# Optimization experiments

Measured on AMD Instinct MI355X. Metric: run time of the kernel, lower is better.

Reference implementation:

```python
import jax, jax.numpy as jnp
import numpy as np

B, S, HID = 4, 2048, 1024
H, DH = 16, 64  # HID = H * DH
ADP, NTASKS = 64, 10
GATE_S = 100.0  # s (soft gate temperature), != smax=400 so no hard threshold


def setup_inputs() -> dict:
    key = jax.random.key(0)
    ks = jax.random.split(key, 13)
    sc = 0.02
    return {
        "hidden_states": jax.random.normal(ks[0], (B, S, HID), jnp.float32),
        "Wq": jax.random.normal(ks[1], (HID, HID), jnp.float32) * sc,
        "bq": jax.random.normal(ks[2], (HID,), jnp.float32) * sc,
        "Wk": jax.random.normal(ks[3], (HID, HID), jnp.float32) * sc,
        "bk": jax.random.normal(ks[4], (HID,), jnp.float32) * sc,
        "Wv": jax.random.normal(ks[5], (HID, HID), jnp.float32) * sc,
        "bv": jax.random.normal(ks[6], (HID,), jnp.float32) * sc,
        "fc1_w": jax.random.normal(ks[7], (HID, ADP), jnp.float32) * sc,
        "fc1_b": jax.random.normal(ks[8], (ADP,), jnp.float32) * sc,
        "fc2_w": jax.random.normal(ks[9], (ADP, HID), jnp.float32) * sc,
        "fc2_b": jax.random.normal(ks[10], (HID,), jnp.float32) * sc,
        "efc1": jax.random.normal(ks[11], (NTASKS, ADP), jnp.float32),
        "efc2": jax.random.normal(ks[12], (NTASKS, HID), jnp.float32),
        "t": 3,
    }


def reference(hidden_states, Wq, bq, Wk, bk, Wv, bv,
              fc1_w, fc1_b, fc2_w, fc2_b, efc1, efc2, t):
    x = hidden_states
    # --- parallel adapter with task gates (add_residual=False) ---
    gfc1 = jax.nn.sigmoid(GATE_S * efc1[t])  # [ADP]
    gfc2 = jax.nn.sigmoid(GATE_S * efc2[t])  # [HID]
    h = jax.nn.relu(x @ fc1_w + fc1_b) * gfc1          # [B,S,ADP]
    adapter_out = jax.nn.relu(h @ fc2_w + fc2_b) * gfc2  # [B,S,HID]
    # --- multi-head self-attention (absolute positions, no mask, eval dropout) ---
    def split_heads(y):  # [B,S,HID] -> [B,H,S,DH]
        return y.reshape(B, S, H, DH).transpose(0, 2, 1, 3)
    q = split_heads(x @ Wq + bq)
    k = split_heads(x @ Wk + bk)
    v = split_heads(x @ Wv + bv)
    scores = jnp.einsum("bhqd,bhkd->bhqk", q, k) / np.sqrt(DH).astype(jnp.float32)
    probs = jax.nn.softmax(scores, axis=-1)
    ctx = jnp.einsum("bhqk,bhkd->bhqd", probs, v)
    ctx = ctx.transpose(0, 2, 1, 3).reshape(B, S, HID)
    return ctx + adapter_out
```

## Files before the change

kernel.cpp:

```cpp
#include <hip/hip_runtime.h>
#include <stdint.h>
#include <stddef.h>

typedef unsigned short u16;
typedef unsigned int u32;
typedef __bf16 bf16x8 __attribute__((ext_vector_type(8)));
typedef __bf16 bf16x4 __attribute__((ext_vector_type(4)));
typedef short s16x4 __attribute__((ext_vector_type(4)));
typedef float f32x4 __attribute__((ext_vector_type(4)));

#define BB  4
#define SS  2048
#define HIDD 1024
#define NH  16
#define DHD 64

#define GLD16(gaddr, laddr) \
  __builtin_amdgcn_global_load_lds( \
      (const __attribute__((address_space(1))) u32*)(gaddr), \
      (__attribute__((address_space(3))) u32*)(laddr), 16, 0, 0)

#define LDS_BARRIER() asm volatile("s_waitcnt lgkmcnt(0)\n\ts_barrier" ::: "memory")

#if __has_builtin(__builtin_amdgcn_exp2f)
  #define EXP2(x) __builtin_amdgcn_exp2f(x)
#else
  #define EXP2(x) __expf((x) * 0.6931471805599453f)
#endif

__device__ __forceinline__ u16 f2b(float f){
  union { float f; unsigned u; } c; c.f = f;
  unsigned r = c.u + 0x7fffu + ((c.u >> 16) & 1u);
  return (u16)(r >> 16);
}
__device__ __forceinline__ f32x4 mfma32(bf16x8 a, bf16x8 b, f32x4 c){
  return __builtin_amdgcn_mfma_f32_16x16x32_bf16(a, b, c, 0, 0, 0);
}
__device__ __forceinline__ f32x4 mfma16(s16x4 a, s16x4 b, f32x4 c){
  return __builtin_amdgcn_mfma_f32_16x16x16bf16_1k(a, b, c, 0, 0, 0);
}

__global__ __launch_bounds__(256)
void prep(const float* __restrict__ x, u16* __restrict__ xb,
          const float* __restrict__ Wq, const float* __restrict__ Wk,
          const float* __restrict__ Wv, const float* __restrict__ f1w,
          const float* __restrict__ f2w,
          u16* __restrict__ wqkv, u16* __restrict__ wtf1, u16* __restrict__ wtf2)
{
  __shared__ float tile[32][33];
  int blk = blockIdx.x;
  const int tid = threadIdx.x;
  if (blk < 8192) {
    int i = blk * 1024 + tid * 4;
    float4 v = *reinterpret_cast<const float4*>(&x[i]);
    ushort4 o;
    o.x = f2b(v.x); o.y = f2b(v.y); o.z = f2b(v.z); o.w = f2b(v.w);
    *reinterpret_cast<ushort4*>(&xb[i]) = o;
    return;
  }
  blk -= 8192;
  if (blk >= 3200) {
    u16* pad = wqkv + (size_t)3136 * 1024;
    uint4 z = make_uint4(0u, 0u, 0u, 0u);
    *reinterpret_cast<uint4*>(&pad[(size_t)(blk - 3200) * 2048 + tid * 8]) = z;
    return;
  }
  const float* in; u16* out; int R, C, c0, r0;
  if (blk < 3072) {
    int m = blk >> 10, t = blk & 1023;
    in = (m == 0) ? Wq : (m == 1) ? Wk : Wv;
    out = wqkv + (size_t)m * 1024 * 1024;
    R = 1024; C = 1024; c0 = (t & 31) * 32; r0 = (t >> 5) * 32;
  } else if (blk < 3136) {
    int t = blk - 3072;
    in = f1w; out = wtf1; R = 1024; C = 64;
    c0 = (t & 1) * 32; r0 = (t >> 1) * 32;
  } else {
    int t = blk - 3136;
    in = f2w; out = wtf2; R = 64; C = 1024;
    c0 = (t & 31) * 32; r0 = (t >> 5) * 32;
  }
  int tx = tid & 31, ty = tid >> 5;
  #pragma unroll
  for (int j = 0; j < 32; j += 8)
    tile[ty + j][tx] = in[(size_t)(r0 + ty + j) * C + c0 + tx];
  __syncthreads();
  #pragma unroll
  for (int j = 0; j < 32; j += 8)
    out[(size_t)(c0 + ty + j) * R + r0 + tx] = f2b(tile[tx][ty + j]);
}

__global__ __launch_bounds__(256)
void gemm_qkv(const u16* __restrict__ X, const u16* __restrict__ Wt,
              const float* __restrict__ bq, const float* __restrict__ bk,
              const float* __restrict__ bv,
              const float* __restrict__ f1b, const float* __restrict__ efc1,
              const int* __restrict__ tptr,
              u16* __restrict__ qb, u16* __restrict__ kb, u16* __restrict__ vt,
              u16* __restrict__ hb)
{
  constexpr int K = 1024;
  __shared__ __align__(16) u16 ldsX[128 * 32];
  __shared__ __align__(16) u16 ldsW[128 * 32];
  const int tid = threadIdx.x;
  const int w = tid >> 6, lane = tid & 63, quad = lane >> 4, ln = lane & 15;
  const int m0 = blockIdx.y * 128, n0 = blockIdx.x * 128;
  const int wrow = (w >> 1) * 64;
  const int wcol = (w & 1) * 64;
  const int srow = tid >> 2;
  const int scol = (tid & 3) * 8;

  f32x4 acc[4][4] = {};

  for (int k0 = 0; k0 < K; k0 += 32) {
    #pragma unroll
    for (int c = 0; c < 2; ++c)
      GLD16(&X[(size_t)(m0 + c * 64 + srow) * K + k0 + scol], &ldsX[c * 2048 + w * 512]);
    #pragma unroll
    for (int c = 0; c < 2; ++c)
      GLD16(&Wt[(size_t)(n0 + c * 64 + srow) * K + k0 + scol], &ldsW[c * 2048 + w * 512]);
    __syncthreads();

    bf16x8 a[4], bfr[4];
    #pragma unroll
    for (int mt = 0; mt < 4; ++mt)
      a[mt] = *reinterpret_cast<const bf16x8*>(&ldsX[(wrow + mt * 16 + ln) * 32 + quad * 8]);
    #pragma unroll
    for (int nt = 0; nt < 4; ++nt)
      bfr[nt] = *reinterpret_cast<const bf16x8*>(&ldsW[(wcol + nt * 16 + ln) * 32 + quad * 8]);
    #pragma unroll
    for (int mt = 0; mt < 4; ++mt)
      #pragma unroll
      for (int nt = 0; nt < 4; ++nt)
        acc[mt][nt] = mfma32(a[mt], bfr[nt], acc[mt][nt]);
    __syncthreads();
  }

  if (n0 < 2048) {
    const float scale = (n0 < 1024) ? 0.18033688f : 1.f;
    const float* bias = (n0 < 1024) ? bq : bk;
    u16* dst = (n0 < 1024) ? qb : kb;
    const int nb = n0 & 1023;
    #pragma unroll
    for (int nt = 0; nt < 4; ++nt) {
      const int col = nb + wcol + nt * 16 + ln;
      const float bvv = bias[col];
      #pragma unroll
      for (int mt = 0; mt < 4; ++mt)
        #pragma unroll
        for (int r = 0; r < 4; ++r) {
          int row = m0 + wrow + mt * 16 + quad * 4 + r;
          dst[(size_t)row * 1024 + col] = f2b((acc[mt][nt][r] + bvv) * scale);
        }
    }
  } else if (n0 < 3072) {
    #pragma unroll
    for (int nt = 0; nt < 4; ++nt) {
      const int colv = (n0 - 2048) + wcol + nt * 16 + ln;
      const float bvv = bv[colv];
      const int h = colv >> 6, d = colv & 63;
      #pragma unroll
      for (int mt = 0; mt < 4; ++mt) {
        int row = m0 + wrow + mt * 16 + quad * 4;
        int bb = row >> 11, s = row & 2047;
        ushort4 o;
        o.x = f2b(acc[mt][nt][0] + bvv);
        o.y = f2b(acc[mt][nt][1] + bvv);
        o.z = f2b(acc[mt][nt][2] + bvv);
        o.w = f2b(acc[mt][nt][3] + bvv);
        *reinterpret_cast<ushort4*>(
            &vt[((((size_t)bb * NH + h) * DHD + d) << 11) + s]) = o;
      }
    }
  } else if (wcol == 0) {
    int t = tptr[0];
    if ((unsigned)t > 9u) t = 0;
    #pragma unroll
    for (int nt = 0; nt < 4; ++nt) {
      const int col = nt * 16 + ln;
      const float bvv = f1b[col];
      const float g = 1.f / (1.f + __expf(-100.f * efc1[t * 64 + col]));
      #pragma unroll
      for (int mt = 0; mt < 4; ++mt)
        #pragma unroll
        for (int r = 0; r < 4; ++r) {
          int row = m0 + wrow + mt * 16 + quad * 4 + r;
          hb[(size_t)row * 64 + col] = f2b(fmaxf(acc[mt][nt][r] + bvv, 0.f) * g);
        }
    }
  }
}

__global__ __launch_bounds__(256, 4)
void attn(const u16* __restrict__ Q, const u16* __restrict__ Kb,
          const u16* __restrict__ Vt, const u16* __restrict__ hb,
          const u16* __restrict__ w2, const float* __restrict__ b2,
          const float* __restrict__ gate2, const int* __restrict__ tptr,
          float* __restrict__ out)
{
  __shared__ __align__(16) u16 ldsK[64 * 72];
  __shared__ __align__(16) u16 ldsV[64 * 76];

  const int tid = threadIdx.x;
  const int w = tid >> 6, lane = tid & 63, quad = lane >> 4, ln = lane & 15;
  const int h = blockIdx.x, b = blockIdx.y, qt = blockIdx.z;
  const int bh = b * NH + h;
  const int qbase = qt * 128 + w * 32;
  const int skey = tid >> 3;
  const int sd   = (tid & 7) * 8;

  bf16x8 qf[2][2];
  #pragma unroll
  for (int q2 = 0; q2 < 2; ++q2)
    #pragma unroll
    for (int kk = 0; kk < 2; ++kk)
      qf[q2][kk] = *reinterpret_cast<const bf16x8*>(
          &Q[(size_t)(b * SS + qbase + q2 * 16 + ln) * HIDD + h * DHD + kk * 32 + quad * 8]);

  f32x4 o[4][2] = {};
  f32x4 lacc[2] = {};
  const s16x4 ones = {0x3F80, 0x3F80, 0x3F80, 0x3F80};

  const u16* Kp = &Kb[(size_t)(b * SS + skey) * HIDD + h * DHD + sd];
  const u16* Vp = &Vt[((size_t)bh * DHD + skey) * SS + sd];

  uint4 rK0 = *reinterpret_cast<const uint4*>(Kp);
  uint4 rK1 = *reinterpret_cast<const uint4*>(Kp + (size_t)32 * HIDD);
  uint4 rV0 = *reinterpret_cast<const uint4*>(Vp);
  uint4 rV1 = *reinterpret_cast<const uint4*>(Vp + (size_t)32 * SS);

  for (int kt = 0; kt < SS; kt += 64) {
    LDS_BARRIER();
    *reinterpret_cast<uint4*>(&ldsK[skey * 72 + sd])        = rK0;
    *reinterpret_cast<uint4*>(&ldsK[(32 + skey) * 72 + sd]) = rK1;
    *reinterpret_cast<uint4*>(&ldsV[skey * 76 + sd])        = rV0;
    *reinterpret_cast<uint4*>(&ldsV[(32 + skey) * 76 + sd]) = rV1;
    if (kt + 64 < SS) {
      const u16* Kn = Kp + (size_t)(kt + 64) * HIDD;
      const u16* Vn = Vp + (kt + 64);
      rK0 = *reinterpret_cast<const uint4*>(Kn);
      rK1 = *reinterpret_cast<const uint4*>(Kn + (size_t)32 * HIDD);
      rV0 = *reinterpret_cast<const uint4*>(Vn);
      rV1 = *reinterpret_cast<const uint4*>(Vn + (size_t)32 * SS);
    }
    LDS_BARRIER();

    f32x4 s[4][2];
    __builtin_amdgcn_s_setprio(1);
    #pragma unroll
    for (int k4 = 0; k4 < 4; ++k4) {
      bf16x8 kf0 = *reinterpret_cast<const bf16x8*>(&ldsK[(k4 * 16 + ln) * 72 + quad * 8]);
      bf16x8 kf1 = *reinterpret_cast<const bf16x8*>(&ldsK[(k4 * 16 + ln) * 72 + 32 + quad * 8]);
      #pragma unroll
      for (int q2 = 0; q2 < 2; ++q2) {
        f32x4 z = {0.f, 0.f, 0.f, 0.f};
        z = mfma32(kf0, qf[q2][0], z);
        z = mfma32(kf1, qf[q2][1], z);
        s[k4][q2] = z;
      }
    }
    __builtin_amdgcn_s_setprio(0);

    s16x4 p[4][2];
    #pragma unroll
    for (int k4 = 0; k4 < 4; ++k4)
      #pragma unroll
      for (int q2 = 0; q2 < 2; ++q2) {
        union { bf16x4 b; s16x4 s; } cv;
        #pragma unroll
        for (int r = 0; r < 4; ++r)
          cv.b[r] = (__bf16)EXP2(s[k4][q2][r]);
        p[k4][q2] = cv.s;
      }

    __builtin_amdgcn_s_setprio(1);
    #pragma unroll
    for (int dt = 0; dt < 4; ++dt) {
      #pragma unroll
      for (int ks = 0; ks < 4; ++ks) {
        s16x4 vf = *reinterpret_cast<const s16x4*>(
            &ldsV[(dt * 16 + ln) * 76 + ks * 16 + quad * 4]);
        #pragma unroll
        for (int q2 = 0; q2 < 2; ++q2)
          o[dt][q2] = mfma16(vf, p[ks][q2], o[dt][q2]);
      }
    }
    #pragma unroll
    for (int ks = 0; ks < 4; ++ks)
      #pragma unroll
      for (int q2 = 0; q2 < 2; ++q2)
        lacc[q2] = mfma16(ones, p[ks][q2], lacc[q2]);
    __builtin_amdgcn_s_setprio(0);
  }

  float rl[2];
  #pragma unroll
  for (int q2 = 0; q2 < 2; ++q2)
    rl[q2] = 1.f / lacc[q2][0];

  f32x4 acc2[4][2] = {};
  #pragma unroll
  for (int kk = 0; kk < 2; ++kk) {
    bf16x8 hf[2];
    #pragma unroll
    for (int q2 = 0; q2 < 2; ++q2) {
      int q = qbase + q2 * 16 + ln;
      hf[q2] = *reinterpret_cast<const bf16x8*>(
          &hb[(size_t)(b * SS + q) * 64 + kk * 32 + quad * 8]);
    }
    #pragma unroll
    for (int dt = 0; dt < 4; ++dt) {
      bf16x8 wf = *reinterpret_cast<const bf16x8*>(
          &w2[(size_t)(h * DHD + dt * 16 + ln) * 64 + kk * 32 + quad * 8]);
      #pragma unroll
      for (int q2 = 0; q2 < 2; ++q2)
        acc2[dt][q2] = mfma32(wf, hf[q2], acc2[dt][q2]);
    }
  }

  int t = tptr[0];
  if ((unsigned)t > 9u) t = 0;
  float bv2[4][4], gv2[4][4];
  #pragma unroll
  for (int dt = 0; dt < 4; ++dt)
    #pragma unroll
    for (int r = 0; r < 4; ++r) {
      int col = h * DHD + dt * 16 + quad * 4 + r;
      bv2[dt][r] = b2[col];
      gv2[dt][r] = 1.f / (1.f + __expf(-100.f * gate2[t * HIDD + col]));
    }

  #pragma unroll
  for (int q2 = 0; q2 < 2; ++q2) {
    const int q = qbase + q2 * 16 + ln;
    float* orow = &out[(size_t)(b * SS + q) * HIDD + h * DHD];
    #pragma unroll
    for (int dt = 0; dt < 4; ++dt)
      #pragma unroll
      for (int r = 0; r < 4; ++r) {
        int d = dt * 16 + quad * 4 + r;
        float ad = fmaxf(acc2[dt][q2][r] + bv2[dt][r], 0.f) * gv2[dt][r];
        orow[d] = o[dt][q2][r] * rl[q2] + ad;
      }
  }
}

extern "C" void kernel_launch(void* const* d_in, const int* in_sizes, int n_in,
                              void* d_out, int out_size, void* d_ws, size_t ws_size,
                              hipStream_t stream) {
  const float* x    = (const float*)d_in[0];
  const float* Wq   = (const float*)d_in[1];
  const float* bq   = (const float*)d_in[2];
  const float* Wk   = (const float*)d_in[3];
  const float* bk   = (const float*)d_in[4];
  const float* Wv   = (const float*)d_in[5];
  const float* bv   = (const float*)d_in[6];
  const float* f1w  = (const float*)d_in[7];
  const float* f1b  = (const float*)d_in[8];
  const float* f2w  = (const float*)d_in[9];
  const float* f2b_ = (const float*)d_in[10];
  const float* efc1 = (const float*)d_in[11];
  const float* efc2 = (const float*)d_in[12];
  const int*   tptr = (const int*)d_in[13];
  float* out = (float*)d_out;

  unsigned char* ws = (unsigned char*)d_ws;
  u16* xb   = (u16*)(ws + 0);
  u16* wqkv = (u16*)(ws + (16u << 20));
  u16* wtf1 = wqkv + (size_t)3072 * 1024;
  u16* wtf2 = (u16*)(ws + (22u << 20) + (256u << 10));
  u16* hb   = (u16*)(ws + (23u << 20));
  u16* qb   = (u16*)(ws + (24u << 20));
  u16* kb   = (u16*)(ws + (40u << 20));
  u16* vt   = (u16*)(ws + (56u << 20));

  prep<<<dim3(11424), 256, 0, stream>>>(x, xb, Wq, Wk, Wv, f1w, f2w,
                                        wqkv, wtf1, wtf2);

  gemm_qkv<<<dim3(25, 64), 256, 0, stream>>>(xb, wqkv, bq, bk, bv,
                                             f1b, efc1, tptr, qb, kb, vt, hb);

  attn<<<dim3(NH, BB, SS / 128), 256, 0, stream>>>(
      qb, kb, vt, hb, wtf2, f2b_, efc2, tptr, out);
}
```

Measured before the change: 292.1 us.

## Double-buffer QKV GEMM LDS loads with swizzle, XCD block remap and priority

Restructures the QKV projection GEMM main loop to double-buffer LDS tiles (K step 64, split into two halves) so global-to-LDS loads of the next tile overlap MFMA work on the current one, using vmcnt-based waits instead of full syncthreads. It adds an XOR swizzle on LDS column groups to reduce bank conflicts, remaps a 1D grid so consecutive blocks across XCDs share tiles for L2 reuse, and raises wave priority around the MFMA block. This increases LDS use fourfold and adds an occupancy hint, which may limit resident blocks.

Measured after the change: 300.3 us. 2.8% more time.

```diff
diff --git a/kernel.cpp b/kernel.cpp
--- a/kernel.cpp
+++ b/kernel.cpp
@@ -21,6 +21,8 @@
       (__attribute__((address_space(3))) u32*)(laddr), 16, 0, 0)
 
 #define LDS_BARRIER() asm volatile("s_waitcnt lgkmcnt(0)\n\ts_barrier" ::: "memory")
+
+#define VMB(n) asm volatile("s_waitcnt vmcnt(" #n ")\n\ts_barrier" ::: "memory")
 
 #if __has_builtin(__builtin_amdgcn_exp2f)
   #define EXP2(x) __builtin_amdgcn_exp2f(x)
@@ -90,7 +92,7 @@
     out[(size_t)(c0 + ty + j) * R + r0 + tx] = f2b(tile[tx][ty + j]);
 }
 
-__global__ __launch_bounds__(256)
+__global__ __launch_bounds__(256, 4)
 void gemm_qkv(const u16* __restrict__ X, const u16* __restrict__ Wt,
               const float* __restrict__ bq, const float* __restrict__ bk,
               const float* __restrict__ bv,
@@ -100,41 +102,63 @@
               u16* __restrict__ hb)
 {
   constexpr int K = 1024;
-  __shared__ __align__(16) u16 ldsX[128 * 32];
-  __shared__ __align__(16) u16 ldsW[128 * 32];
+  __shared__ __align__(16) u16 ldsX[2][2][128 * 32];
+  __shared__ __align__(16) u16 ldsW[2][2][128 * 32];
   const int tid = threadIdx.x;
   const int w = tid >> 6, lane = tid & 63, quad = lane >> 4, ln = lane & 15;
-  const int m0 = blockIdx.y * 128, n0 = blockIdx.x * 128;
+  const int id = blockIdx.x;
+  const int swzb = (id & 7) * 200 + (id >> 3);
+  const int m0 = (swzb / 25) * 128;
+  const int n0 = (swzb % 25) * 128;
   const int wrow = (w >> 1) * 64;
   const int wcol = (w & 1) * 64;
-  const int srow = tid >> 2;
-  const int scol = (tid & 3) * 8;
+
+  const int trow = tid >> 2;
+  const int cgo  = (((tid & 3) ^ ((tid >> 2) & 3) ^ ((tid >> 4) & 3)) * 8);
+  const u16* Xs = X  + (size_t)(m0 + trow) * K + cgo;
+  const u16* Ws = Wt + (size_t)(n0 + trow) * K + cgo;
+
+  #define STAGE(d, kt, kh) do { \
+    GLD16(Xs + (size_t)(kt) * 64 + (kh) * 32,                  &ldsX[d][kh][w * 512]); \
+    GLD16(Xs + (size_t)64 * K + (size_t)(kt) * 64 + (kh) * 32, &ldsX[d][kh][2048 + w * 512]); \
+    GLD16(Ws + (size_t)(kt) * 64 + (kh) * 32,                  &ldsW[d][kh][w * 512]); \
+    GLD16(Ws + (size_t)64 * K + (size_t)(kt) * 64 + (kh) * 32, &ldsW[d][kh][2048 + w * 512]); \
+  } while (0)
+
+  const int cA = (quad ^ (ln & 3) ^ ((ln >> 2) & 3)) * 8;
 
   f32x4 acc[4][4] = {};
 
-  for (int k0 = 0; k0 < K; k0 += 32) {
-    #pragma unroll
-    for (int c = 0; c < 2; ++c)
-      GLD16(&X[(size_t)(m0 + c * 64 + srow) * K + k0 + scol], &ldsX[c * 2048 + w * 512]);
-    #pragma unroll
-    for (int c = 0; c < 2; ++c)
-      GLD16(&Wt[(size_t)(n0 + c * 64 + srow) * K + k0 + scol], &ldsW[c * 2048 + w * 512]);
-    __syncthreads();
-
-    bf16x8 a[4], bfr[4];
-    #pragma unroll
-    for (int mt = 0; mt < 4; ++mt)
-      a[mt] = *reinterpret_cast<const bf16x8*>(&ldsX[(wrow + mt * 16 + ln) * 32 + quad * 8]);
-    #pragma unroll
-    for (int nt = 0; nt < 4; ++nt)
-      bfr[nt] = *reinterpret_cast<const bf16x8*>(&ldsW[(wcol + nt * 16 + ln) * 32 + quad * 8]);
-    #pragma unroll
-    for (int mt = 0; mt < 4; ++mt)
+  STAGE(0, 0, 0);
+  STAGE(0, 0, 1);
+  VMB(4);
+
+  for (int kt = 0; kt < 16; ++kt) {
+    const int d = kt & 1;
+    #pragma unroll
+    for (int kh = 0; kh < 2; ++kh) {
+      if (kt + 1 < 16) STAGE(d ^ 1, kt + 1, kh);
+      bf16x8 a[4], bfr[4];
+      #pragma unroll
+      for (int mt = 0; mt < 4; ++mt)
+        a[mt] = *reinterpret_cast<const bf16x8*>(
+            &ldsX[d][kh][(wrow + mt * 16 + ln) * 32 + cA]);
       #pragma unroll
       for (int nt = 0; nt < 4; ++nt)
-        acc[mt][nt] = mfma32(a[mt], bfr[nt], acc[mt][nt]);
-    __syncthreads();
-  }
+        bfr[nt] = *reinterpret_cast<const bf16x8*>(
+            &ldsW[d][kh][(wcol + nt * 16 + ln) * 32 + cA]);
+      __builtin_amdgcn_s_setprio(1);
+      #pragma unroll
+      for (int mt = 0; mt < 4; ++mt)
+        #pragma unroll
+        for (int nt = 0; nt < 4; ++nt)
+          acc[mt][nt] = mfma32(a[mt], bfr[nt], acc[mt][nt]);
+      __builtin_amdgcn_s_setprio(0);
+      if (kt + 1 < 16)      VMB(4);
+      else if (kh == 0)     VMB(0);
+    }
+  }
+  #undef STAGE
 
   if (n0 < 2048) {
     const float scale = (n0 < 1024) ? 0.18033688f : 1.f;
@@ -158,7 +182,7 @@
     for (int nt = 0; nt < 4; ++nt) {
       const int colv = (n0 - 2048) + wcol + nt * 16 + ln;
       const float bvv = bv[colv];
-      const int h = colv >> 6, d = colv & 63;
+      const int h = colv >> 6, d2 = colv & 63;
       #pragma unroll
       for (int mt = 0; mt < 4; ++mt) {
         int row = m0 + wrow + mt * 16 + quad * 4;
@@ -169,7 +193,7 @@
         o.z = f2b(acc[mt][nt][2] + bvv);
         o.w = f2b(acc[mt][nt][3] + bvv);
         *reinterpret_cast<ushort4*>(
-            &vt[((((size_t)bb * NH + h) * DHD + d) << 11) + s]) = o;
+            &vt[((((size_t)bb * NH + h) * DHD + d2) << 11) + s]) = o;
       }
     }
   } else if (wcol == 0) {
@@ -377,8 +401,8 @@
   prep<<<dim3(11424), 256, 0, stream>>>(x, xb, Wq, Wk, Wv, f1w, f2w,
                                         wqkv, wtf1, wtf2);
 
-  gemm_qkv<<<dim3(25, 64), 256, 0, stream>>>(xb, wqkv, bq, bk, bv,
-                                             f1b, efc1, tptr, qb, kb, vt, hb);
+  gemm_qkv<<<dim3(1600), 256, 0, stream>>>(xb, wqkv, bq, bk, bv,
+                                           f1b, efc1, tptr, qb, kb, vt, hb);
 
   attn<<<dim3(NH, BB, SS / 128), 256, 0, stream>>>(
       qb, kb, vt, hb, wtf2, f2b_, efc2, tptr, out);
```

## Triple-buffer QKV GEMM with 128x256 tiles and swizzled 1D grid

Applied to the files above, without the earlier changes.

Rewrites the fused QKV/fc1 GEMM to use a three-stage LDS ring with global_load_lds prefetch two k-steps ahead, replacing the two-barrier-per-iteration loop with vmcnt waits. Tile width doubles to 256 columns per block (each wave computes 64x128), and the grid becomes 1D with an XCD-aware swizzle, padding the fc1 columns so N=3328. The aim is to hide global latency and improve reuse of A tiles and L2 locality, at the cost of more registers and LDS, which lowers occupancy. The prep kernel and workspace are resized to hold the extra padded weight rows.

After: 276.4 us, median of 2. 1.06x faster.

```diff
diff --git a/kernel.cpp b/kernel.cpp
--- a/kernel.cpp
+++ b/kernel.cpp
@@ -21,6 +21,8 @@
       (__attribute__((address_space(3))) u32*)(laddr), 16, 0, 0)
 
 #define LDS_BARRIER() asm volatile("s_waitcnt lgkmcnt(0)\n\ts_barrier" ::: "memory")
+
+#define VMB(n) asm volatile("s_waitcnt vmcnt(" #n ")\n\ts_barrier" ::: "memory")
 
 #if __has_builtin(__builtin_amdgcn_exp2f)
   #define EXP2(x) __builtin_amdgcn_exp2f(x)
@@ -90,7 +92,7 @@
     out[(size_t)(c0 + ty + j) * R + r0 + tx] = f2b(tile[tx][ty + j]);
 }
 
-__global__ __launch_bounds__(256)
+__global__ __launch_bounds__(256, 2)
 void gemm_qkv(const u16* __restrict__ X, const u16* __restrict__ Wt,
               const float* __restrict__ bq, const float* __restrict__ bk,
               const float* __restrict__ bv,
@@ -100,41 +102,63 @@
               u16* __restrict__ hb)
 {
   constexpr int K = 1024;
-  __shared__ __align__(16) u16 ldsX[128 * 32];
-  __shared__ __align__(16) u16 ldsW[128 * 32];
+  __shared__ __align__(16) u16 ldsA[3][128 * 32];
+  __shared__ __align__(16) u16 ldsB[3][256 * 32];
   const int tid = threadIdx.x;
   const int w = tid >> 6, lane = tid & 63, quad = lane >> 4, ln = lane & 15;
-  const int m0 = blockIdx.y * 128, n0 = blockIdx.x * 128;
+  const int id = blockIdx.x;
+  const int swz = (id & 7) * 104 + (id >> 3);
+  const int m0 = (swz / 13) * 128;
+  const int n0 = (swz % 13) * 256;
   const int wrow = (w >> 1) * 64;
-  const int wcol = (w & 1) * 64;
-  const int srow = tid >> 2;
-  const int scol = (tid & 3) * 8;
-
-  f32x4 acc[4][4] = {};
-
-  for (int k0 = 0; k0 < K; k0 += 32) {
-    #pragma unroll
-    for (int c = 0; c < 2; ++c)
-      GLD16(&X[(size_t)(m0 + c * 64 + srow) * K + k0 + scol], &ldsX[c * 2048 + w * 512]);
-    #pragma unroll
-    for (int c = 0; c < 2; ++c)
-      GLD16(&Wt[(size_t)(n0 + c * 64 + srow) * K + k0 + scol], &ldsW[c * 2048 + w * 512]);
-    __syncthreads();
-
-    bf16x8 a[4], bfr[4];
+  const int wcol = (w & 1) * 128;
+
+  const u16* Xs = X  + (size_t)(m0 + w * 32 + (lane >> 2)) * K + (lane & 3) * 8;
+  const u16* Ws = Wt + (size_t)(n0 + w * 64 + (lane >> 2)) * K + (lane & 3) * 8;
+
+  #define STAGE(buf, kk) do { \
+    GLD16(Xs + (size_t)(kk),            &ldsA[buf][w * 1024]); \
+    GLD16(Xs + (size_t)16 * K + (kk),   &ldsA[buf][w * 1024 + 512]); \
+    GLD16(Ws + (size_t)(kk),            &ldsB[buf][w * 2048]); \
+    GLD16(Ws + (size_t)16 * K + (kk),   &ldsB[buf][w * 2048 + 512]); \
+    GLD16(Ws + (size_t)32 * K + (kk),   &ldsB[buf][w * 2048 + 1024]); \
+    GLD16(Ws + (size_t)48 * K + (kk),   &ldsB[buf][w * 2048 + 1536]); \
+  } while (0)
+
+  f32x4 acc[4][8] = {};
+
+  STAGE(0, 0);
+  STAGE(1, 32);
+  VMB(6);
+
+  int cur = 0;
+  for (int t = 0; t < 32; ++t) {
+    if (t + 2 < 32) {
+      int sb = cur + 2; if (sb >= 3) sb -= 3;
+      STAGE(sb, (t + 2) * 32);
+    }
+
+    bf16x8 a[4], b[8];
     #pragma unroll
     for (int mt = 0; mt < 4; ++mt)
-      a[mt] = *reinterpret_cast<const bf16x8*>(&ldsX[(wrow + mt * 16 + ln) * 32 + quad * 8]);
-    #pragma unroll
-    for (int nt = 0; nt < 4; ++nt)
-      bfr[nt] = *reinterpret_cast<const bf16x8*>(&ldsW[(wcol + nt * 16 + ln) * 32 + quad * 8]);
+      a[mt] = *reinterpret_cast<const bf16x8*>(
+          &ldsA[cur][(wrow + mt * 16 + ln) * 32 + quad * 8]);
+    #pragma unroll
+    for (int nt = 0; nt < 8; ++nt)
+      b[nt] = *reinterpret_cast<const bf16x8*>(
+          &ldsB[cur][(wcol + nt * 16 + ln) * 32 + quad * 8]);
     #pragma unroll
     for (int mt = 0; mt < 4; ++mt)
       #pragma unroll
-      for (int nt = 0; nt < 4; ++nt)
-        acc[mt][nt] = mfma32(a[mt], bfr[nt], acc[mt][nt]);
-    __syncthreads();
-  }
+      for (int nt = 0; nt < 8; ++nt)
+        acc[mt][nt] = mfma32(a[mt], b[nt], acc[mt][nt]);
+
+    if (t + 2 < 32)      VMB(6);
+    else if (t == 30)    VMB(0);
+
+    cur = (cur + 1 == 3) ? 0 : cur + 1;
+  }
+  #undef STAGE
 
   if (n0 < 2048) {
     const float scale = (n0 < 1024) ? 0.18033688f : 1.f;
@@ -142,7 +166,7 @@
     u16* dst = (n0 < 1024) ? qb : kb;
     const int nb = n0 & 1023;
     #pragma unroll
-    for (int nt = 0; nt < 4; ++nt) {
+    for (int nt = 0; nt < 8; ++nt) {
       const int col = nb + wcol + nt * 16 + ln;
       const float bvv = bias[col];
       #pragma unroll
@@ -155,10 +179,10 @@
     }
   } else if (n0 < 3072) {
     #pragma unroll
-    for (int nt = 0; nt < 4; ++nt) {
+    for (int nt = 0; nt < 8; ++nt) {
       const int colv = (n0 - 2048) + wcol + nt * 16 + ln;
       const float bvv = bv[colv];
-      const int h = colv >> 6, d = colv & 63;
+      const int h = colv >> 6, d2 = colv & 63;
       #pragma unroll
       for (int mt = 0; mt < 4; ++mt) {
         int row = m0 + wrow + mt * 16 + quad * 4;
@@ -169,10 +193,10 @@
         o.z = f2b(acc[mt][nt][2] + bvv);
         o.w = f2b(acc[mt][nt][3] + bvv);
         *reinterpret_cast<ushort4*>(
-            &vt[((((size_t)bb * NH + h) * DHD + d) << 11) + s]) = o;
+            &vt[((((size_t)bb * NH + h) * DHD + d2) << 11) + s]) = o;
       }
     }
-  } else if (wcol == 0) {
+  } else if ((w & 1) == 0) {
     int t = tptr[0];
     if ((unsigned)t > 9u) t = 0;
     #pragma unroll
@@ -368,17 +392,17 @@
   u16* xb   = (u16*)(ws + 0);
   u16* wqkv = (u16*)(ws + (16u << 20));
   u16* wtf1 = wqkv + (size_t)3072 * 1024;
-  u16* wtf2 = (u16*)(ws + (22u << 20) + (256u << 10));
+  u16* wtf2 = (u16*)(ws + (22u << 20) + (512u << 10));
   u16* hb   = (u16*)(ws + (23u << 20));
   u16* qb   = (u16*)(ws + (24u << 20));
   u16* kb   = (u16*)(ws + (40u << 20));
   u16* vt   = (u16*)(ws + (56u << 20));
 
-  prep<<<dim3(11424), 256, 0, stream>>>(x, xb, Wq, Wk, Wv, f1w, f2w,
+  prep<<<dim3(11488), 256, 0, stream>>>(x, xb, Wq, Wk, Wv, f1w, f2w,
                                         wqkv, wtf1, wtf2);
 
-  gemm_qkv<<<dim3(25, 64), 256, 0, stream>>>(xb, wqkv, bq, bk, bv,
-                                             f1b, efc1, tptr, qb, kb, vt, hb);
+  gemm_qkv<<<dim3(832), 256, 0, stream>>>(xb, wqkv, bq, bk, bv,
+                                          f1b, efc1, tptr, qb, kb, vt, hb);
 
   attn<<<dim3(NH, BB, SS / 128), 256, 0, stream>>>(
       qb, kb, vt, hb, wtf2, f2b_, efc2, tptr, out);
```

## Rework QKV GEMM with 256x256 tiles, double-buffered swizzled LDS, and block remap

Applied to the files above, without the earlier changes.

Rewrites the fused QKV/fc1 projection GEMM so each 512-thread block computes a 256x256 output tile with BK=64 instead of a 128x128 tile with BK=32. LDS is now double-buffered, so the next k-tile's global-to-LDS loads overlap the current tile's MFMAs with one barrier per iteration. LDS chunks are XOR-swizzled to avoid bank conflicts, and a 1D grid with block-id remapping improves L2 reuse. The N padding grows to 3328 columns, so the workspace layout and prep grid change to match. The cost is about 128KB of LDS and heavy register use per block, which limits the CU to one block and adds wasted padded columns.

Result: faster. 279.1 us (-4.5%).

```diff
diff --git a/kernel.cpp b/kernel.cpp
--- a/kernel.cpp
+++ b/kernel.cpp
@@ -21,6 +21,8 @@
       (__attribute__((address_space(3))) u32*)(laddr), 16, 0, 0)
 
 #define LDS_BARRIER() asm volatile("s_waitcnt lgkmcnt(0)\n\ts_barrier" ::: "memory")
+
+#define VMB(n) asm volatile("s_waitcnt vmcnt(" #n ")\n\ts_barrier" ::: "memory")
 
 #if __has_builtin(__builtin_amdgcn_exp2f)
   #define EXP2(x) __builtin_amdgcn_exp2f(x)
@@ -90,7 +92,7 @@
     out[(size_t)(c0 + ty + j) * R + r0 + tx] = f2b(tile[tx][ty + j]);
 }
 
-__global__ __launch_bounds__(256)
+__global__ __launch_bounds__(512, 2)
 void gemm_qkv(const u16* __restrict__ X, const u16* __restrict__ Wt,
               const float* __restrict__ bq, const float* __restrict__ bk,
               const float* __restrict__ bv,
@@ -100,53 +102,92 @@
               u16* __restrict__ hb)
 {
   constexpr int K = 1024;
-  __shared__ __align__(16) u16 ldsX[128 * 32];
-  __shared__ __align__(16) u16 ldsW[128 * 32];
+  __shared__ __align__(16) u16 ldsA[2][256 * 64];
+  __shared__ __align__(16) u16 ldsB[2][256 * 64];
   const int tid = threadIdx.x;
   const int w = tid >> 6, lane = tid & 63, quad = lane >> 4, ln = lane & 15;
-  const int m0 = blockIdx.y * 128, n0 = blockIdx.x * 128;
-  const int wrow = (w >> 1) * 64;
-  const int wcol = (w & 1) * 64;
-  const int srow = tid >> 2;
-  const int scol = (tid & 3) * 8;
-
-  f32x4 acc[4][4] = {};
-
-  for (int k0 = 0; k0 < K; k0 += 32) {
-    #pragma unroll
-    for (int c = 0; c < 2; ++c)
-      GLD16(&X[(size_t)(m0 + c * 64 + srow) * K + k0 + scol], &ldsX[c * 2048 + w * 512]);
-    #pragma unroll
-    for (int c = 0; c < 2; ++c)
-      GLD16(&Wt[(size_t)(n0 + c * 64 + srow) * K + k0 + scol], &ldsW[c * 2048 + w * 512]);
-    __syncthreads();
-
-    bf16x8 a[4], bfr[4];
+  const int id = blockIdx.x;
+  const int swz = (id & 7) * 52 + (id >> 3);
+  const int m0 = (swz / 13) * 256;
+  const int n0 = (swz % 13) * 256;
+  const int wrow = (w >> 2) * 128;
+  const int wcol = (w & 3) * 64;
+
+  const int srow = lane >> 3;
+  const int schunk = (lane & 7) ^ srow;
+  const u16* Xs = X  + (size_t)(m0 + w * 32 + srow) * K + schunk * 8;
+  const u16* Ws = Wt + (size_t)(n0 + w * 32 + srow) * K + schunk * 8;
+
+  #define STAGE_TILE(buf, kt) do { \
+    GLD16(Xs + (size_t)(kt),            &ldsA[buf][(w * 32 +  0) * 64]); \
+    GLD16(Xs + (size_t) 8 * K + (kt),   &ldsA[buf][(w * 32 +  8) * 64]); \
+    GLD16(Xs + (size_t)16 * K + (kt),   &ldsA[buf][(w * 32 + 16) * 64]); \
+    GLD16(Xs + (size_t)24 * K + (kt),   &ldsA[buf][(w * 32 + 24) * 64]); \
+    GLD16(Ws + (size_t)(kt),            &ldsB[buf][(w * 32 +  0) * 64]); \
+    GLD16(Ws + (size_t) 8 * K + (kt),   &ldsB[buf][(w * 32 +  8) * 64]); \
+    GLD16(Ws + (size_t)16 * K + (kt),   &ldsB[buf][(w * 32 + 16) * 64]); \
+    GLD16(Ws + (size_t)24 * K + (kt),   &ldsB[buf][(w * 32 + 24) * 64]); \
+  } while (0)
+
+  f32x4 acc[8][4] = {};
+
+  STAGE_TILE(0, 0);
+  VMB(0);
+
+  for (int t = 0; t < 16; ++t) {
+    const int rb = t & 1;
+    if (t + 1 < 16) STAGE_TILE(rb ^ 1, (t + 1) * 64);
+
+    bf16x8 a0[4][2], a1[4][2], b0[2][2], b1[2][2];
     #pragma unroll
     for (int mt = 0; mt < 4; ++mt)
-      a[mt] = *reinterpret_cast<const bf16x8*>(&ldsX[(wrow + mt * 16 + ln) * 32 + quad * 8]);
-    #pragma unroll
-    for (int nt = 0; nt < 4; ++nt)
-      bfr[nt] = *reinterpret_cast<const bf16x8*>(&ldsW[(wcol + nt * 16 + ln) * 32 + quad * 8]);
-    #pragma unroll
-    for (int mt = 0; mt < 4; ++mt)
-      #pragma unroll
-      for (int nt = 0; nt < 4; ++nt)
-        acc[mt][nt] = mfma32(a[mt], bfr[nt], acc[mt][nt]);
-    __syncthreads();
-  }
+      #pragma unroll
+      for (int kk = 0; kk < 2; ++kk) {
+        a0[mt][kk] = *reinterpret_cast<const bf16x8*>(
+            &ldsA[rb][(wrow + mt * 16 + ln) * 64 + (((kk * 4 + quad) ^ (ln & 7)) * 8)]);
+        a1[mt][kk] = *reinterpret_cast<const bf16x8*>(
+            &ldsA[rb][(wrow + 64 + mt * 16 + ln) * 64 + (((kk * 4 + quad) ^ (ln & 7)) * 8)]);
+      }
+    #pragma unroll
+    for (int nt = 0; nt < 2; ++nt)
+      #pragma unroll
+      for (int kk = 0; kk < 2; ++kk) {
+        b0[nt][kk] = *reinterpret_cast<const bf16x8*>(
+            &ldsB[rb][(wcol + nt * 16 + ln) * 64 + (((kk * 4 + quad) ^ (ln & 7)) * 8)]);
+        b1[nt][kk] = *reinterpret_cast<const bf16x8*>(
+            &ldsB[rb][(wcol + 32 + nt * 16 + ln) * 64 + (((kk * 4 + quad) ^ (ln & 7)) * 8)]);
+      }
+
+    __builtin_amdgcn_s_setprio(1);
+    #pragma unroll
+    for (int kk = 0; kk < 2; ++kk) {
+      #pragma unroll
+      for (int mt = 0; mt < 4; ++mt)
+        #pragma unroll
+        for (int nt = 0; nt < 2; ++nt) {
+          acc[mt][nt]         = mfma32(a0[mt][kk], b0[nt][kk], acc[mt][nt]);
+          acc[mt][2 + nt]     = mfma32(a0[mt][kk], b1[nt][kk], acc[mt][2 + nt]);
+          acc[4 + mt][2 + nt] = mfma32(a1[mt][kk], b1[nt][kk], acc[4 + mt][2 + nt]);
+          acc[4 + mt][nt]     = mfma32(a1[mt][kk], b0[nt][kk], acc[4 + mt][nt]);
+        }
+    }
+    __builtin_amdgcn_s_setprio(0);
+
+    VMB(0);
+  }
+  #undef STAGE_TILE
 
   if (n0 < 2048) {
     const float scale = (n0 < 1024) ? 0.18033688f : 1.f;
     const float* bias = (n0 < 1024) ? bq : bk;
     u16* dst = (n0 < 1024) ? qb : kb;
-    const int nb = n0 & 1023;
+    const int nb = (n0 & 1023) + wcol;
     #pragma unroll
     for (int nt = 0; nt < 4; ++nt) {
-      const int col = nb + wcol + nt * 16 + ln;
+      const int col = nb + nt * 16 + ln;
       const float bvv = bias[col];
       #pragma unroll
-      for (int mt = 0; mt < 4; ++mt)
+      for (int mt = 0; mt < 8; ++mt)
         #pragma unroll
         for (int r = 0; r < 4; ++r) {
           int row = m0 + wrow + mt * 16 + quad * 4 + r;
@@ -158,9 +199,9 @@
     for (int nt = 0; nt < 4; ++nt) {
       const int colv = (n0 - 2048) + wcol + nt * 16 + ln;
       const float bvv = bv[colv];
-      const int h = colv >> 6, d = colv & 63;
-      #pragma unroll
-      for (int mt = 0; mt < 4; ++mt) {
+      const int h = colv >> 6, d2 = colv & 63;
+      #pragma unroll
+      for (int mt = 0; mt < 8; ++mt) {
         int row = m0 + wrow + mt * 16 + quad * 4;
         int bb = row >> 11, s = row & 2047;
         ushort4 o;
@@ -169,7 +210,7 @@
         o.z = f2b(acc[mt][nt][2] + bvv);
         o.w = f2b(acc[mt][nt][3] + bvv);
         *reinterpret_cast<ushort4*>(
-            &vt[((((size_t)bb * NH + h) * DHD + d) << 11) + s]) = o;
+            &vt[((((size_t)bb * NH + h) * DHD + d2) << 11) + s]) = o;
       }
     }
   } else if (wcol == 0) {
@@ -181,7 +222,7 @@
       const float bvv = f1b[col];
       const float g = 1.f / (1.f + __expf(-100.f * efc1[t * 64 + col]));
       #pragma unroll
-      for (int mt = 0; mt < 4; ++mt)
+      for (int mt = 0; mt < 8; ++mt)
         #pragma unroll
         for (int r = 0; r < 4; ++r) {
           int row = m0 + wrow + mt * 16 + quad * 4 + r;
@@ -368,17 +409,17 @@
   u16* xb   = (u16*)(ws + 0);
   u16* wqkv = (u16*)(ws + (16u << 20));
   u16* wtf1 = wqkv + (size_t)3072 * 1024;
-  u16* wtf2 = (u16*)(ws + (22u << 20) + (256u << 10));
+  u16* wtf2 = (u16*)(ws + (22u << 20) + (512u << 10));
   u16* hb   = (u16*)(ws + (23u << 20));
   u16* qb   = (u16*)(ws + (24u << 20));
   u16* kb   = (u16*)(ws + (40u << 20));
   u16* vt   = (u16*)(ws + (56u << 20));
 
-  prep<<<dim3(11424), 256, 0, stream>>>(x, xb, Wq, Wk, Wv, f1w, f2w,
+  prep<<<dim3(11488), 256, 0, stream>>>(x, xb, Wq, Wk, Wv, f1w, f2w,
                                         wqkv, wtf1, wtf2);
 
-  gemm_qkv<<<dim3(25, 64), 256, 0, stream>>>(xb, wqkv, bq, bk, bv,
-                                             f1b, efc1, tptr, qb, kb, vt, hb);
+  gemm_qkv<<<dim3(416), 512, 0, stream>>>(xb, wqkv, bq, bk, bv,
+                                          f1b, efc1, tptr, qb, kb, vt, hb);
 
   attn<<<dim3(NH, BB, SS / 128), 256, 0, stream>>>(
       qb, kb, vt, hb, wtf2, f2b_, efc2, tptr, out);
```
